# Optimization experiments

Measured on AMD Instinct MI355X. Metric: run time of the kernel, lower is better.

## Reference

```python
import jax, jax.numpy as jnp
import numpy as np

T = 2048        # num tokens
HID = 2048      # hidden_size
HQ = 16         # num_heads
HKV = 8         # num_kv_heads
D = 128         # head_dim
P = 2           # power retention exponent
THETA = 10000.0 # rope base
SCALE = D ** -0.5


def setup_inputs() -> dict:
    key = jax.random.key(0)
    ks = jax.random.split(key, 8)
    s = 0.02
    return {
        "positions": jnp.arange(T, dtype=jnp.int64) if jax.config.jax_enable_x64 else jnp.arange(T, dtype=jnp.int32),
        "hidden_states": jax.random.normal(ks[0], (T, HID), jnp.float32),
        "Wq": jax.random.normal(ks[1], (HID, HQ * D), jnp.float32) * s,
        "bq": jnp.zeros((HQ * D,), jnp.float32),
        "Wk": jax.random.normal(ks[2], (HID, HKV * D), jnp.float32) * s,
        "bk": jnp.zeros((HKV * D,), jnp.float32),
        "Wv": jax.random.normal(ks[3], (HID, HKV * D), jnp.float32) * s,
        "bv": jnp.zeros((HKV * D,), jnp.float32),
        "Wg": jax.random.normal(ks[4], (HID, HKV), jnp.float32) * s,
        "bg": jnp.zeros((HKV,), jnp.float32),
        "Wo": jax.random.normal(ks[5], (HQ * D, HID), jnp.float32) * s,
        "bo": jnp.zeros((HID,), jnp.float32),
    }


def _rope_neox(x, pos):
    # x: [T, H, D], pos: [T]; rotate-half (neox) style, rotary_dim == head_dim
    half = D // 2
    inv_freq = 1.0 / (THETA ** (jnp.arange(0, D, 2, dtype=jnp.float32) / D))  # [D/2]
    freqs = pos.astype(jnp.float32)[:, None] * inv_freq                        # [T, D/2]
    cos = jnp.cos(freqs)[:, None, :]
    sin = jnp.sin(freqs)[:, None, :]
    x1, x2 = x[..., :half], x[..., half:]
    return jnp.concatenate([x1 * cos - x2 * sin, x2 * cos + x1 * sin], axis=-1)


def reference(positions, hidden_states, Wq, bq, Wk, bk, Wv, bv, Wg, bg, Wo, bo):
    # QKVG projections
    q = (hidden_states @ Wq + bq).reshape(T, HQ, D)
    k = (hidden_states @ Wk + bk).reshape(T, HKV, D)
    v = (hidden_states @ Wv + bv).reshape(T, HKV, D)
    g = hidden_states @ Wg + bg            # [T, HKV], one gate scalar per kv head

    # RoPE on q/k, logsigmoid gate in fp32
    q = _rope_neox(q, positions)
    k = _rope_neox(k, positions)
    g = jax.nn.log_sigmoid(g.astype(jnp.float32))   # [T, HKV], <= 0
    G = jnp.cumsum(g, axis=0)                       # [T, HKV] cumulative log-decay

    # GQA: expand kv heads to query heads
    rep = HQ // HKV
    k = jnp.repeat(k, rep, axis=1)   # [T, HQ, D]
    v = jnp.repeat(v, rep, axis=1)
    G = jnp.repeat(G, rep, axis=1)   # [T, HQ]

    # Power retention (quadratic attention form, seq_len <= switch_over_seq_len):
    # W_ij = (scale * q_i . k_j)^p * exp(G_i - G_j), causal j <= i
    S = jnp.einsum('thd,shd->hts', q, k) * SCALE      # [H, T, T]
    S = S ** P
    Gh = G.T                                          # [H, T]
    mask = jnp.tril(jnp.ones((T, T), dtype=bool))
    diff = jnp.where(mask[None], Gh[:, :, None] - Gh[:, None, :], -jnp.inf)
    W = S * jnp.exp(diff)                             # decay<=1 inside mask, 0 outside

    out = jnp.einsum('hts,shd->thd', W, v)            # [T, H, D]
    out = out.reshape(T, HQ * D) @ Wo + bo            # o_proj
    return out
```

## Files before the change

kernel.cpp:

```cpp
#include <hip/hip_runtime.h>
#include <hip/hip_bf16.h>
#include <math.h>

#define T_SEQ 2048
#define HID 2048
#define HQ 16
#define HKV 8
#define D_HEAD 128
#define HALF 64
#define SCALE_F 0.08838834764831845f
#define PROJW 4096

typedef __attribute__((ext_vector_type(8))) short bf16x8;
typedef __attribute__((ext_vector_type(4))) float f32x4;

static __device__ __forceinline__ short f2bf(float x) {
  unsigned u = __builtin_bit_cast(unsigned, x);
  unsigned r = (u + 0x7FFF + ((u >> 16) & 1)) >> 16;
  return (short)r;
}
static __device__ __forceinline__ float bf2f(unsigned short u) {
  unsigned v = ((unsigned)u) << 16;
  return __builtin_bit_cast(float, v);
}

#define GLDS(gsrc, ldst) \
  __builtin_amdgcn_global_load_lds((const __attribute__((address_space(1))) void*)(gsrc), \
                                   (__attribute__((address_space(3))) void*)(ldst), 16, 0, 0)

__global__ __launch_bounds__(256)
void transpose_all(const float* __restrict__ Wq, const float* __restrict__ Wk,
                   const float* __restrict__ Wv, const float* __restrict__ Wo,
                   short* __restrict__ BTall, short* __restrict__ WoT)
{
  const int bx = blockIdx.x;
  const int k0 = blockIdx.y * 32;
  const float* src; short* dst; int Nsrc, n0;
  if (bx < 64)       { src = Wq; Nsrc = 2048; dst = BTall;                       n0 = bx * 32; }
  else if (bx < 96)  { src = Wk; Nsrc = 1024; dst = BTall + (size_t)2048 * 2048; n0 = (bx - 64) * 32; }
  else if (bx < 128) { src = Wv; Nsrc = 1024; dst = BTall + (size_t)3072 * 2048; n0 = (bx - 96) * 32; }
  else               { src = Wo; Nsrc = 2048; dst = WoT;                         n0 = (bx - 128) * 32; }

  __shared__ float tile[32][33];
  const int r = threadIdx.x >> 5, c = threadIdx.x & 31;
  #pragma unroll
  for (int i = 0; i < 4; ++i)
    tile[r + i * 8][c] = src[(size_t)(k0 + r + i * 8) * Nsrc + n0 + c];
  __syncthreads();
  const int n = threadIdx.x >> 3, k4 = (threadIdx.x & 7) * 4;
  short4 o;
  o.x = f2bf(tile[k4 + 0][n]); o.y = f2bf(tile[k4 + 1][n]);
  o.z = f2bf(tile[k4 + 2][n]); o.w = f2bf(tile[k4 + 3][n]);
  *reinterpret_cast<short4*>(&dst[(size_t)(n0 + n) * 2048 + k0 + k4]) = o;
}

__global__ __launch_bounds__(256)
void add_f32(float* __restrict__ out, const float* __restrict__ part, int n4)
{
  int i = blockIdx.x * blockDim.x + threadIdx.x;
  if (i >= n4) return;
  float4 a = reinterpret_cast<float4*>(out)[i];
  const float4 b = reinterpret_cast<const float4*>(part)[i];
  a.x += b.x; a.y += b.y; a.z += b.z; a.w += b.w;
  reinterpret_cast<float4*>(out)[i] = a;
}

template <bool OBF>
__global__ __launch_bounds__(256, 1)
void gemmF(const short* __restrict__ A, const short* __restrict__ BT,
           const float* __restrict__ b0, const float* __restrict__ b1,
           const float* __restrict__ b2, int s1, int s2,
           void* __restrict__ Cout0, void* __restrict__ Cout1,
           int N, int Kst, int klen)
{
  __shared__ short Al[3][256 * 64];
  __shared__ short Bl[3][128 * 64];
  const int tid = threadIdx.x, wid = tid >> 6, lane = tid & 63;
  const int z = blockIdx.z;
  const int koff = z * klen;
  const int nwg = gridDim.x * gridDim.y;
  const int orig = blockIdx.y * gridDim.x + blockIdx.x;
  const int swz = (orig & 7) * (nwg >> 3) + (orig >> 3);
  const int bx = swz % gridDim.x, by = swz / gridDim.x;
  const int bm0 = by * 256, bn0 = bx * 128;
  const int wr = wid >> 1, wc = wid & 1;
  const int c = lane & 15, g = lane >> 4;
  const int xc = (c & 7) << 4;
  const int nk = klen >> 6;

  f32x4 acc[8][4] = {};

#define STGA(p, kt, j) do {                                                   \
    const int cid = (j) * 256 + tid;                                          \
    const int rr = cid >> 3;                                                  \
    const int gx = (cid & 7) ^ (rr & 7);                                      \
    GLDS(A + (size_t)(bm0 + rr) * Kst + koff + (kt) * 64 + gx * 8,            \
         (char*)&Al[p][0] + ((j) * 256 + wid * 64) * 16);                     \
  } while (0)
#define STGB(p, kt, j) do {                                                   \
    const int cid = (j) * 256 + tid;                                          \
    const int rr = cid >> 3;                                                  \
    const int gx = (cid & 7) ^ (rr & 7);                                      \
    GLDS(BT + (size_t)(bn0 + rr) * Kst + koff + (kt) * 64 + gx * 8,           \
         (char*)&Bl[p][0] + ((j) * 256 + wid * 64) * 16);                     \
  } while (0)
#define STAGE(p, kt) do {                                                     \
    STGA(p, kt, 0); STGA(p, kt, 1); STGA(p, kt, 2); STGA(p, kt, 3);           \
    STGA(p, kt, 4); STGA(p, kt, 5); STGA(p, kt, 6); STGA(p, kt, 7);           \
    STGB(p, kt, 0); STGB(p, kt, 1); STGB(p, kt, 2); STGB(p, kt, 3);           \
  } while (0)

#define RDA(p, mf, ks)                                                        \
  (*reinterpret_cast<const bf16x8*>((const char*)&Al[p][0] +                  \
      (size_t)(wr * 128 + (mf) * 16 + c) * 128 + (((ks) * 64 + g * 16) ^ xc)))
#define RDB(p, nf, ks)                                                        \
  (*reinterpret_cast<const bf16x8*>((const char*)&Bl[p][0] +                  \
      (size_t)(wc * 64 + (nf) * 16 + c) * 128 + (((ks) * 64 + g * 16) ^ xc)))

  STAGE(0, 0);
  if (nk > 1) {
    STAGE(1, 1);
    asm volatile("s_waitcnt vmcnt(12)" ::: "memory");
  } else {
    asm volatile("s_waitcnt vmcnt(0)" ::: "memory");
  }
  __builtin_amdgcn_s_barrier();
  __builtin_amdgcn_sched_barrier(0);

  for (int t = 0; t < nk; ++t) {
    const int p = t % 3, sb = (t + 2) % 3;
    if (t + 2 < nk) STAGE(sb, t + 2);

    bf16x8 a0[8], br0[4];
    #pragma unroll
    for (int mf = 0; mf < 8; ++mf) a0[mf] = RDA(p, mf, 0);
    #pragma unroll
    for (int nf = 0; nf < 4; ++nf) br0[nf] = RDB(p, nf, 0);
    asm volatile("s_waitcnt lgkmcnt(0)" ::: "memory");
    __builtin_amdgcn_sched_barrier(0);

    bf16x8 a1[8], br1[4];
    #pragma unroll
    for (int mf = 0; mf < 8; ++mf) a1[mf] = RDA(p, mf, 1);
    #pragma unroll
    for (int nf = 0; nf < 4; ++nf) br1[nf] = RDB(p, nf, 1);
    __builtin_amdgcn_sched_barrier(0);

    __builtin_amdgcn_s_setprio(1);
    #pragma unroll
    for (int mf = 0; mf < 8; ++mf)
      #pragma unroll
      for (int nf = 0; nf < 4; ++nf)
        acc[mf][nf] = __builtin_amdgcn_mfma_f32_16x16x32_bf16(a0[mf], br0[nf], acc[mf][nf], 0, 0, 0);
    __builtin_amdgcn_s_setprio(0);

    asm volatile("s_waitcnt lgkmcnt(0)" ::: "memory");
    __builtin_amdgcn_sched_barrier(0);

    __builtin_amdgcn_s_setprio(1);
    #pragma unroll
    for (int mf = 0; mf < 8; ++mf)
      #pragma unroll
      for (int nf = 0; nf < 4; ++nf)
        acc[mf][nf] = __builtin_amdgcn_mfma_f32_16x16x32_bf16(a1[mf], br1[nf], acc[mf][nf], 0, 0, 0);
    __builtin_amdgcn_s_setprio(0);

    if (t + 1 < nk) {
      __builtin_amdgcn_sched_barrier(0);
      if (t + 2 < nk) asm volatile("s_waitcnt vmcnt(12)" ::: "memory");
      else            asm volatile("s_waitcnt vmcnt(0)" ::: "memory");
      __builtin_amdgcn_s_barrier();
      __builtin_amdgcn_sched_barrier(0);
    }
  }

  void* Cout = z ? Cout1 : Cout0;
  const int crow = bm0 + wr * 128 + g * 4;
  const int ccol = bn0 + wc * 64 + c;
  #pragma unroll
  for (int nf = 0; nf < 4; ++nf) {
    const int col = ccol + nf * 16;
    float b = 0.f;
    if (z == 0)
      b = (col < s1) ? b0[col] : ((col < s2) ? b1[col - s1] : b2[col - s2]);
    #pragma unroll
    for (int mf = 0; mf < 8; ++mf)
      #pragma unroll
      for (int r = 0; r < 4; ++r) {
        const int row = crow + mf * 16 + r;
        const float v = acc[mf][nf][r] + b;
        if constexpr (OBF)
          ((short*)Cout)[(size_t)row * N + col] = f2bf(v);
        else
          ((float*)Cout)[(size_t)row * N + col] = v;
      }
  }
#undef STGA
#undef STGB
#undef STAGE
#undef RDA
#undef RDB
}

__global__ __launch_bounds__(256)
void gproj_kernel(const float* __restrict__ hs, const float* __restrict__ Wg,
                  const float* __restrict__ bg, float* __restrict__ gT,
                  short* __restrict__ hsb)
{
  const int t = blockIdx.x, tid = threadIdx.x;
  __shared__ float red[256][9];
  float a[8] = {0.f, 0.f, 0.f, 0.f, 0.f, 0.f, 0.f, 0.f};
  for (int cc = tid; cc < HID; cc += 256) {
    const float hv = hs[(size_t)t * HID + cc];
    hsb[(size_t)t * HID + cc] = f2bf(hv);
    const float4 w0 = *reinterpret_cast<const float4*>(Wg + (size_t)cc * 8);
    const float4 w1 = *reinterpret_cast<const float4*>(Wg + (size_t)cc * 8 + 4);
    a[0] = fmaf(hv, w0.x, a[0]); a[1] = fmaf(hv, w0.y, a[1]);
    a[2] = fmaf(hv, w0.z, a[2]); a[3] = fmaf(hv, w0.w, a[3]);
    a[4] = fmaf(hv, w1.x, a[4]); a[5] = fmaf(hv, w1.y, a[5]);
    a[6] = fmaf(hv, w1.z, a[6]); a[7] = fmaf(hv, w1.w, a[7]);
  }
  #pragma unroll
  for (int j = 0; j < 8; ++j) red[tid][j] = a[j];
  __syncthreads();
  for (int s = 128; s >= 1; s >>= 1) {
    if (tid < s) {
      #pragma unroll
      for (int j = 0; j < 8; ++j) red[tid][j] += red[tid + s][j];
    }
    __syncthreads();
  }
  if (tid < 8) {
    const float x = red[0][tid] + bg[tid];
    const float nx = -x;
    const float sp = (nx > 20.f) ? nx : log1pf(expf(nx));
    gT[(size_t)tid * T_SEQ + t] = -sp;
  }
}

__global__ __launch_bounds__(512)
void gscan_kernel(const float* __restrict__ gT, float* __restrict__ Gct)
{
  const int h = blockIdx.x;
  const int tid = threadIdx.x;
  const int wid = tid >> 6, lane = tid & 63;
  __shared__ float wsum[8];

  const float4 v = reinterpret_cast<const float4*>(gT + (size_t)h * T_SEQ)[tid];
  const float p0 = v.x, p1 = p0 + v.y, p2 = p1 + v.z, p3 = p2 + v.w;

  float sc = p3;
  #pragma unroll
  for (int off = 1; off < 64; off <<= 1) {
    const float o = __shfl_up(sc, off, 64);
    if (lane >= off) sc += o;
  }
  if (lane == 63) wsum[wid] = sc;
  __syncthreads();
  float wof = 0.f;
  #pragma unroll
  for (int w = 0; w < 8; ++w) wof += (w < wid) ? wsum[w] : 0.f;

  const float excl = wof + sc - p3;
  reinterpret_cast<float4*>(Gct + (size_t)h * T_SEQ)[tid] =
      make_float4(excl + p0, excl + p1, excl + p2, excl + p3);
}

__global__ __launch_bounds__(256)
void rope_vtrans(short* __restrict__ proj, unsigned short* __restrict__ vt)
{
  __shared__ float cs[64], sn[64];
  __shared__ unsigned short tile[32][33];

  if (blockIdx.x < 2048) {
    const int t = blockIdx.x;
    if (threadIdx.x < 64) {
      const int i = threadIdx.x;
      const float f = (float)t * powf(10000.0f, -(float)i / 64.0f);
      cs[i] = cosf(f); sn[i] = sinf(f);
    }
    __syncthreads();
    const int u = threadIdx.x;
    if (u < 192) {
      const int hh = u >> 3, ch = u & 7;
      short* base = proj + (size_t)t * PROJW +
                    ((hh < HQ) ? hh * D_HEAD : 2048 + (hh - HQ) * D_HEAD);
      bf16x8 x1 = *reinterpret_cast<bf16x8*>(base + ch * 8);
      bf16x8 x2 = *reinterpret_cast<bf16x8*>(base + HALF + ch * 8);
      #pragma unroll
      for (int j = 0; j < 8; ++j) {
        const float a = bf2f((unsigned short)x1[j]);
        const float b = bf2f((unsigned short)x2[j]);
        const float cc = cs[ch * 8 + j], ss = sn[ch * 8 + j];
        x1[j] = f2bf(a * cc - b * ss);
        x2[j] = f2bf(b * cc + a * ss);
      }
      *reinterpret_cast<bf16x8*>(base + ch * 8) = x1;
      *reinterpret_cast<bf16x8*>(base + HALF + ch * 8) = x2;
    }
  } else {
    const int idx = blockIdx.x - 2048;
    const int tt = (idx & 63) * 32, dd = ((idx >> 6) & 3) * 32, hk = idx >> 8;
    const unsigned short* pj = (const unsigned short*)proj;
    const int c = threadIdx.x & 31, r0 = (threadIdx.x >> 5) * 4;
    #pragma unroll
    for (int i = 0; i < 4; ++i)
      tile[r0 + i][c] = pj[(size_t)(tt + r0 + i) * PROJW + 3072 + hk * 128 + dd + c];
    __syncthreads();
    #pragma unroll
    for (int i = 0; i < 4; ++i)
      vt[(size_t)(hk * 128 + dd + r0 + i) * T_SEQ + tt + c] = tile[c][r0 + i];
  }
}

__global__ __launch_bounds__(256, 1)
void attn_mfma(const short* __restrict__ proj, const short* __restrict__ vt,
               const float* __restrict__ Gct, short* __restrict__ outb)
{
  __shared__ __align__(16) char smem[86528];
  const int hk = blockIdx.x;
  const int tb = blockIdx.y * 64;
  const int tid = threadIdx.x;
  const int wid = tid >> 6, lane = tid & 63;
  const int c = lane & 15, g = lane >> 4;
  const int h = 2 * hk + (wid >> 1);
  const int tw = tb + (wid & 1) * 32;
  const float* Gh = Gct + (size_t)hk * T_SEQ;

  const float glim = Gh[tb] + 90.0f;
  int lo = 0, hi = tb;
  while (lo < hi) {
    const int mid = (lo + hi) >> 1;
    if (Gh[mid] > glim) lo = mid + 1; else hi = mid;
  }
  const int sfirst = lo & ~63;
  const int nst = ((tb - sfirst) >> 6) + 1;

  bf16x8 qf[2][4];
  #pragma unroll
  for (int tt = 0; tt < 2; ++tt)
    #pragma unroll
    for (int kb = 0; kb < 4; ++kb)
      qf[tt][kb] = *reinterpret_cast<const bf16x8*>(
          proj + (size_t)(tw + 16 * tt + c) * PROJW + h * D_HEAD + kb * 32 + g * 8);
  const float gt0 = Gh[tw + c];
  const float gt1 = Gh[tw + 16 + c];
  const float gtw = Gh[tw];
  const int twmax = tw + 31;

  f32x4 accv[2][8] = {};

#define ASTG(buf, s64)                                                                   \
  do {                                                                                   \
    _Pragma("unroll")                                                                    \
    for (int i2 = 0; i2 < 4; ++i2) {                                                     \
      const int cid = tid + 256 * i2;                                                    \
      const int kr = cid >> 4, kc = cid & 15;                                            \
      GLDS(proj + (size_t)((s64) + kr) * PROJW + 2048 + hk * 128 + ((kc ^ (kr & 7)) * 8),\
           smem + (buf) * 16384 + cid * 16);                                             \
      const int vr = cid >> 3, vc = cid & 7;                                             \
      GLDS(vt + (size_t)(hk * 128 + vr) * T_SEQ + (s64) + ((vc ^ (vr & 7)) * 8),         \
           smem + 32768 + (buf) * 16384 + cid * 16);                                     \
    }                                                                                    \
    if (tid < 64) ((float*)(smem + 86016))[(buf) * 64 + tid] = Gh[(s64) + tid];          \
  } while (0)

  ASTG(0, sfirst);
  __syncthreads();

  for (int i = 0; i < nst; ++i) {
    const int cur = i & 1;
    if (i + 1 < nst) ASTG(cur ^ 1, sfirst + (i + 1) * 64);
    const int sbase64 = sfirst + i * 64;
    const float* Gss = (const float*)(smem + 86016) + cur * 64;
    char* Pmy = smem + 65536 + wid * 5120;

    #pragma unroll
    for (int st = 0; st < 2; ++st) {
      const int s0 = sbase64 + st * 32;
      if (s0 > twmax) continue;
      if (gtw - Gss[st * 32 + 31] < -90.0f) continue;

      bf16x8 kf[2][4];
      #pragma unroll
      for (int sg = 0; sg < 2; ++sg)
        #pragma unroll
        for (int kb = 0; kb < 4; ++kb) {
          const int row = st * 32 + 16 * sg + c;
          const int byt = (row * 256 + kb * 64 + g * 16) ^ ((c & 7) << 4);
          kf[sg][kb] = *reinterpret_cast<const bf16x8*>(smem + cur * 16384 + byt);
        }
      f32x4 sa[2][2] = {};
      #pragma unroll
      for (int kb = 0; kb < 4; ++kb)
        #pragma unroll
        for (int sg = 0; sg < 2; ++sg)
          #pragma unroll
          for (int tt = 0; tt < 2; ++tt)
            sa[sg][tt] = __builtin_amdgcn_mfma_f32_16x16x32_bf16(
                kf[sg][kb], qf[tt][kb], sa[sg][tt], 0, 0, 0);

      #pragma unroll
      for (int sg = 0; sg < 2; ++sg) {
        const float4 gs = *reinterpret_cast<const float4*>(&Gss[st * 32 + sg * 16 + g * 4]);
        const float gsv[4] = {gs.x, gs.y, gs.z, gs.w};
        #pragma unroll
        for (int tt = 0; tt < 2; ++tt) {
          const int tg = tw + 16 * tt + c;
          const float gt = tt ? gt1 : gt0;
          const int sg0 = s0 + sg * 16 + g * 4;
          float w[4];
          #pragma unroll
          for (int r = 0; r < 4; ++r) {
            const float dv = sa[sg][tt][r] * SCALE_F;
            const float ww = dv * dv * __expf(gt - gsv[r]);
            w[r] = (sg0 + r <= tg) ? ww : 0.0f;
          }
          uint2 pv;
          pv.x = ((unsigned)(unsigned short)f2bf(w[1]) << 16) | (unsigned short)f2bf(w[0]);
          pv.y = ((unsigned)(unsigned short)f2bf(w[3]) << 16) | (unsigned short)f2bf(w[2]);
          *reinterpret_cast<uint2*>(Pmy + st * 2560 + (c + 16 * tt) * 80 + 8 * g + 32 * sg) = pv;
        }
      }
      asm volatile("s_waitcnt lgkmcnt(0)" ::: "memory");
      __builtin_amdgcn_sched_barrier(0);

      bf16x8 pf[2];
      #pragma unroll
      for (int tt = 0; tt < 2; ++tt)
        pf[tt] = *reinterpret_cast<const bf16x8*>(Pmy + st * 2560 + (c + 16 * tt) * 80 + g * 16);

      #pragma unroll
      for (int db = 0; db < 8; ++db) {
        const int row = 16 * db + c;
        const int byt = (row * 128 + st * 64 + g * 16) ^ ((c & 7) << 4);
        const bf16x8 vf = *reinterpret_cast<const bf16x8*>(smem + 32768 + cur * 16384 + byt);
        #pragma unroll
        for (int tt = 0; tt < 2; ++tt)
          accv[tt][db] = __builtin_amdgcn_mfma_f32_16x16x32_bf16(pf[tt], vf, accv[tt][db], 0, 0, 0);
      }
    }
    __syncthreads();
  }

  char* Wme = smem + wid * 8704;
  #pragma unroll
  for (int tt = 0; tt < 2; ++tt)
    #pragma unroll
    for (int db = 0; db < 8; ++db)
      #pragma unroll
      for (int r = 0; r < 4; ++r)
        *reinterpret_cast<short*>(Wme + (16 * tt + 4 * g + r) * 272 + (16 * db + c) * 2)
            = f2bf(accv[tt][db][r]);
  asm volatile("s_waitcnt lgkmcnt(0)" ::: "memory");
  __builtin_amdgcn_sched_barrier(0);
  #pragma unroll
  for (int e = 0; e < 8; ++e) {
    const int idx = e * 64 + lane;
    const int tr = idx >> 4, d0 = (idx & 15) * 8;
    const bf16x8 vv = *reinterpret_cast<const bf16x8*>(Wme + tr * 272 + d0 * 2);
    *reinterpret_cast<bf16x8*>(outb + ((size_t)(tw + tr) * HQ + h) * D_HEAD + d0) = vv;
  }
#undef ASTG
}

extern "C" void kernel_launch(void* const* d_in, const int* in_sizes, int n_in,
                              void* d_out, int out_size, void* d_ws, size_t ws_size,
                              hipStream_t stream)
{
  const float* hs = (const float*)d_in[1];
  const float* Wq = (const float*)d_in[2];
  const float* bq = (const float*)d_in[3];
  const float* Wk = (const float*)d_in[4];
  const float* bk = (const float*)d_in[5];
  const float* Wv = (const float*)d_in[6];
  const float* bv = (const float*)d_in[7];
  const float* Wg = (const float*)d_in[8];
  const float* bg = (const float*)d_in[9];
  const float* Wo = (const float*)d_in[10];
  const float* bo = (const float*)d_in[11];
  float* outp = (float*)d_out;

  short* proj  = (short*)d_ws;
  short* vtb   = proj + (size_t)T_SEQ * PROJW;
  float* gT    = (float*)(vtb + (size_t)HKV * D_HEAD * T_SEQ);
  float* Gct   = gT + 16384;
  short* hsb   = (short*)(Gct + 16384);
  short* BTall = hsb + (size_t)2048 * 2048;
  short* WoT   = BTall + (size_t)4096 * 2048;
  short* attnout = hsb;
  float* opart   = (float*)BTall;

  transpose_all<<<dim3(192, 64), 256, 0, stream>>>(Wq, Wk, Wv, Wo, BTall, WoT);

  gproj_kernel<<<2048, 256, 0, stream>>>(hs, Wg, bg, gT, hsb);
  gscan_kernel<<<8, 512, 0, stream>>>(gT, Gct);

  gemmF<true><<<dim3(32, 8, 1), 256, 0, stream>>>(
      hsb, BTall, bq, bk, bv, 2048, 3072, proj, proj, PROJW, 2048, 2048);

  rope_vtrans<<<4096, 256, 0, stream>>>(proj, (unsigned short*)vtb);

  attn_mfma<<<dim3(8, 32), 256, 0, stream>>>(proj, vtb, Gct, attnout);

  gemmF<false><<<dim3(16, 8, 2), 256, 0, stream>>>(
      attnout, WoT, bo, bo, bo, 1 << 30, 1 << 30, outp, opart, 2048, 2048, 1024);
  add_f32<<<4096, 256, 0, stream>>>(outp, opart, 1048576);
}
```

Measured before the change: 152.5 us.

## Use 256x256 split-K GEMM tiles with bf16 partials and fused fold+RoPE

```diff
diff --git a/kernel.cpp b/kernel.cpp
--- a/kernel.cpp
+++ b/kernel.cpp
@@ -29,17 +29,15 @@
                                    (__attribute__((address_space(3))) void*)(ldst), 16, 0, 0)
 
 __global__ __launch_bounds__(256)
-void transpose_all(const float* __restrict__ Wq, const float* __restrict__ Wk,
-                   const float* __restrict__ Wv, const float* __restrict__ Wo,
-                   short* __restrict__ BTall, short* __restrict__ WoT)
+void transpose_qkvw(const float* __restrict__ Wq, const float* __restrict__ Wk,
+                    const float* __restrict__ Wv, short* __restrict__ BTall)
 {
   const int bx = blockIdx.x;
   const int k0 = blockIdx.y * 32;
   const float* src; short* dst; int Nsrc, n0;
   if (bx < 64)       { src = Wq; Nsrc = 2048; dst = BTall;                       n0 = bx * 32; }
   else if (bx < 96)  { src = Wk; Nsrc = 1024; dst = BTall + (size_t)2048 * 2048; n0 = (bx - 64) * 32; }
-  else if (bx < 128) { src = Wv; Nsrc = 1024; dst = BTall + (size_t)3072 * 2048; n0 = (bx - 96) * 32; }
-  else               { src = Wo; Nsrc = 2048; dst = WoT;                         n0 = (bx - 128) * 32; }
+  else               { src = Wv; Nsrc = 1024; dst = BTall + (size_t)3072 * 2048; n0 = (bx - 96) * 32; }
 
   __shared__ float tile[32][33];
   const int r = threadIdx.x >> 5, c = threadIdx.x & 31;
@@ -55,35 +53,41 @@
 }
 
 __global__ __launch_bounds__(256)
-void add_f32(float* __restrict__ out, const float* __restrict__ part, int n4)
-{
-  int i = blockIdx.x * blockDim.x + threadIdx.x;
-  if (i >= n4) return;
-  float4 a = reinterpret_cast<float4*>(out)[i];
-  const float4 b = reinterpret_cast<const float4*>(part)[i];
-  a.x += b.x; a.y += b.y; a.z += b.z; a.w += b.w;
-  reinterpret_cast<float4*>(out)[i] = a;
-}
-
-template <bool OBF>
-__global__ __launch_bounds__(256, 1)
-void gemmF(const short* __restrict__ A, const short* __restrict__ BT,
-           const float* __restrict__ b0, const float* __restrict__ b1,
-           const float* __restrict__ b2, int s1, int s2,
-           void* __restrict__ Cout0, void* __restrict__ Cout1,
-           int N, int Kst, int klen)
-{
-  __shared__ short Al[3][256 * 64];
-  __shared__ short Bl[3][128 * 64];
+void transpose_wo(const float* __restrict__ Wo, short* __restrict__ WoT)
+{
+  const int k0 = blockIdx.y * 32, n0 = blockIdx.x * 32;
+  __shared__ float tile[32][33];
+  const int r = threadIdx.x >> 5, c = threadIdx.x & 31;
+  #pragma unroll
+  for (int i = 0; i < 4; ++i)
+    tile[r + i * 8][c] = Wo[(size_t)(k0 + r + i * 8) * 2048 + n0 + c];
+  __syncthreads();
+  const int n = threadIdx.x >> 3, k4 = (threadIdx.x & 7) * 4;
+  short4 o;
+  o.x = f2bf(tile[k4 + 0][n]); o.y = f2bf(tile[k4 + 1][n]);
+  o.z = f2bf(tile[k4 + 2][n]); o.w = f2bf(tile[k4 + 3][n]);
+  *reinterpret_cast<short4*>(&WoT[(size_t)(n0 + n) * 2048 + k0 + k4]) = o;
+}
+
+template <bool OBF0>
+__global__ __launch_bounds__(512, 1)
+void gemm256(const short* __restrict__ A, const short* __restrict__ BT,
+             const float* __restrict__ b0, const float* __restrict__ b1,
+             const float* __restrict__ b2, int s1, int s2,
+             void* __restrict__ C0, short* __restrict__ P1,
+             short* __restrict__ P2, short* __restrict__ P3,
+             int N, int Kst, int klen)
+{
+  __shared__ __align__(16) short Al[2][256 * 64];
+  __shared__ __align__(16) short Bl[2][256 * 64];
   const int tid = threadIdx.x, wid = tid >> 6, lane = tid & 63;
-  const int z = blockIdx.z;
-  const int koff = z * klen;
+  const int z = blockIdx.z, koff = z * klen;
   const int nwg = gridDim.x * gridDim.y;
   const int orig = blockIdx.y * gridDim.x + blockIdx.x;
   const int swz = (orig & 7) * (nwg >> 3) + (orig >> 3);
   const int bx = swz % gridDim.x, by = swz / gridDim.x;
-  const int bm0 = by * 256, bn0 = bx * 128;
-  const int wr = wid >> 1, wc = wid & 1;
+  const int bm0 = by * 256, bn0 = bx * 256;
+  const int wr = wid >> 2, wc = wid & 3;
   const int c = lane & 15, g = lane >> 4;
   const int xc = (c & 7) << 4;
   const int nk = klen >> 6;
@@ -91,22 +95,21 @@
   f32x4 acc[8][4] = {};
 
 #define STGA(p, kt, j) do {                                                   \
-    const int cid = (j) * 256 + tid;                                          \
+    const int cid = (j) * 512 + tid;                                          \
     const int rr = cid >> 3;                                                  \
     const int gx = (cid & 7) ^ (rr & 7);                                      \
     GLDS(A + (size_t)(bm0 + rr) * Kst + koff + (kt) * 64 + gx * 8,            \
-         (char*)&Al[p][0] + ((j) * 256 + wid * 64) * 16);                     \
+         (char*)&Al[p][0] + ((j) * 512 + wid * 64) * 16);                     \
   } while (0)
 #define STGB(p, kt, j) do {                                                   \
-    const int cid = (j) * 256 + tid;                                          \
+    const int cid = (j) * 512 + tid;                                          \
     const int rr = cid >> 3;                                                  \
     const int gx = (cid & 7) ^ (rr & 7);                                      \
     GLDS(BT + (size_t)(bn0 + rr) * Kst + koff + (kt) * 64 + gx * 8,           \
-         (char*)&Bl[p][0] + ((j) * 256 + wid * 64) * 16);                     \
+         (char*)&Bl[p][0] + ((j) * 512 + wid * 64) * 16);                     \
   } while (0)
 #define STAGE(p, kt) do {                                                     \
     STGA(p, kt, 0); STGA(p, kt, 1); STGA(p, kt, 2); STGA(p, kt, 3);           \
-    STGA(p, kt, 4); STGA(p, kt, 5); STGA(p, kt, 6); STGA(p, kt, 7);           \
     STGB(p, kt, 0); STGB(p, kt, 1); STGB(p, kt, 2); STGB(p, kt, 3);           \
   } while (0)
 
@@ -118,81 +121,78 @@
       (size_t)(wc * 64 + (nf) * 16 + c) * 128 + (((ks) * 64 + g * 16) ^ xc)))
 
   STAGE(0, 0);
-  if (nk > 1) {
-    STAGE(1, 1);
-    asm volatile("s_waitcnt vmcnt(12)" ::: "memory");
-  } else {
-    asm volatile("s_waitcnt vmcnt(0)" ::: "memory");
-  }
+  asm volatile("s_waitcnt vmcnt(0)" ::: "memory");
   __builtin_amdgcn_s_barrier();
   __builtin_amdgcn_sched_barrier(0);
 
   for (int t = 0; t < nk; ++t) {
-    const int p = t % 3, sb = (t + 2) % 3;
-    if (t + 2 < nk) STAGE(sb, t + 2);
-
-    bf16x8 a0[8], br0[4];
-    #pragma unroll
-    for (int mf = 0; mf < 8; ++mf) a0[mf] = RDA(p, mf, 0);
-    #pragma unroll
-    for (int nf = 0; nf < 4; ++nf) br0[nf] = RDB(p, nf, 0);
-    asm volatile("s_waitcnt lgkmcnt(0)" ::: "memory");
-    __builtin_amdgcn_sched_barrier(0);
-
-    bf16x8 a1[8], br1[4];
-    #pragma unroll
-    for (int mf = 0; mf < 8; ++mf) a1[mf] = RDA(p, mf, 1);
-    #pragma unroll
-    for (int nf = 0; nf < 4; ++nf) br1[nf] = RDB(p, nf, 1);
-    __builtin_amdgcn_sched_barrier(0);
-
-    __builtin_amdgcn_s_setprio(1);
-    #pragma unroll
-    for (int mf = 0; mf < 8; ++mf)
-      #pragma unroll
-      for (int nf = 0; nf < 4; ++nf)
-        acc[mf][nf] = __builtin_amdgcn_mfma_f32_16x16x32_bf16(a0[mf], br0[nf], acc[mf][nf], 0, 0, 0);
-    __builtin_amdgcn_s_setprio(0);
-
-    asm volatile("s_waitcnt lgkmcnt(0)" ::: "memory");
-    __builtin_amdgcn_sched_barrier(0);
-
-    __builtin_amdgcn_s_setprio(1);
-    #pragma unroll
-    for (int mf = 0; mf < 8; ++mf)
-      #pragma unroll
-      for (int nf = 0; nf < 4; ++nf)
-        acc[mf][nf] = __builtin_amdgcn_mfma_f32_16x16x32_bf16(a1[mf], br1[nf], acc[mf][nf], 0, 0, 0);
-    __builtin_amdgcn_s_setprio(0);
+    const int p = t & 1;
+    if (t + 1 < nk) STAGE(p ^ 1, t + 1);
+
+    {
+      bf16x8 af[8], bfr[4];
+      #pragma unroll
+      for (int mf = 0; mf < 8; ++mf) af[mf] = RDA(p, mf, 0);
+      #pragma unroll
+      for (int nf = 0; nf < 4; ++nf) bfr[nf] = RDB(p, nf, 0);
+      asm volatile("s_waitcnt lgkmcnt(0)" ::: "memory");
+      __builtin_amdgcn_sched_barrier(0);
+      __builtin_amdgcn_s_setprio(1);
+      #pragma unroll
+      for (int mf = 0; mf < 8; ++mf)
+        #pragma unroll
+        for (int nf = 0; nf < 4; ++nf)
+          acc[mf][nf] = __builtin_amdgcn_mfma_f32_16x16x32_bf16(af[mf], bfr[nf], acc[mf][nf], 0, 0, 0);
+      __builtin_amdgcn_s_setprio(0);
+    }
+    {
+      bf16x8 af[8], bfr[4];
+      #pragma unroll
+      for (int mf = 0; mf < 8; ++mf) af[mf] = RDA(p, mf, 1);
+      #pragma unroll
+      for (int nf = 0; nf < 4; ++nf) bfr[nf] = RDB(p, nf, 1);
+      asm volatile("s_waitcnt lgkmcnt(0)" ::: "memory");
+      __builtin_amdgcn_sched_barrier(0);
+      __builtin_amdgcn_s_setprio(1);
+      #pragma unroll
+      for (int mf = 0; mf < 8; ++mf)
+        #pragma unroll
+        for (int nf = 0; nf < 4; ++nf)
+          acc[mf][nf] = __builtin_amdgcn_mfma_f32_16x16x32_bf16(af[mf], bfr[nf], acc[mf][nf], 0, 0, 0);
+      __builtin_amdgcn_s_setprio(0);
+    }
 
     if (t + 1 < nk) {
       __builtin_amdgcn_sched_barrier(0);
-      if (t + 2 < nk) asm volatile("s_waitcnt vmcnt(12)" ::: "memory");
-      else            asm volatile("s_waitcnt vmcnt(0)" ::: "memory");
+      asm volatile("s_waitcnt vmcnt(0)" ::: "memory");
       __builtin_amdgcn_s_barrier();
       __builtin_amdgcn_sched_barrier(0);
     }
   }
 
-  void* Cout = z ? Cout1 : Cout0;
-  const int crow = bm0 + wr * 128 + g * 4;
-  const int ccol = bn0 + wc * 64 + c;
+  const int crow = bm0 + wr * 128;
+  const int ccol0 = bn0 + wc * 64;
   #pragma unroll
   for (int nf = 0; nf < 4; ++nf) {
-    const int col = ccol + nf * 16;
+    const int col = ccol0 + nf * 16 + c;
     float b = 0.f;
     if (z == 0)
       b = (col < s1) ? b0[col] : ((col < s2) ? b1[col - s1] : b2[col - s2]);
+    short* P = (z == 1) ? P1 : ((z == 2) ? P2 : P3);
     #pragma unroll
     for (int mf = 0; mf < 8; ++mf)
       #pragma unroll
       for (int r = 0; r < 4; ++r) {
-        const int row = crow + mf * 16 + r;
+        const int row = crow + mf * 16 + g * 4 + r;
         const float v = acc[mf][nf][r] + b;
-        if constexpr (OBF)
-          ((short*)Cout)[(size_t)row * N + col] = f2bf(v);
-        else
-          ((float*)Cout)[(size_t)row * N + col] = v;
+        if (z == 0) {
+          if constexpr (OBF0)
+            ((short*)C0)[(size_t)row * N + col] = f2bf(v);
+          else
+            ((float*)C0)[(size_t)row * N + col] = v;
+        } else {
+          P[(size_t)row * N + col] = f2bf(v);
+        }
       }
   }
 #undef STGA
@@ -267,50 +267,75 @@
 }
 
 __global__ __launch_bounds__(256)
-void rope_vtrans(short* __restrict__ proj, unsigned short* __restrict__ vt)
-{
+void qkv_fold_rope(short* __restrict__ proj, const short* __restrict__ part1)
+{
+  const int t = blockIdx.x;
   __shared__ float cs[64], sn[64];
+  if (threadIdx.x < 64) {
+    const int i = threadIdx.x;
+    const float f = (float)t * powf(10000.0f, -(float)i / 64.0f);
+    cs[i] = cosf(f); sn[i] = sinf(f);
+  }
+  __syncthreads();
+
+  const int ch = ((threadIdx.x >> 3) << 4) + (threadIdx.x & 7);
+  const size_t base = (size_t)t * PROJW + ch * 8;
+  bf16x8 a1 = *reinterpret_cast<bf16x8*>(proj + base);
+  bf16x8 a2 = *reinterpret_cast<bf16x8*>(proj + base + 64);
+  const bf16x8 q1 = *reinterpret_cast<const bf16x8*>(part1 + base);
+  const bf16x8 q2 = *reinterpret_cast<const bf16x8*>(part1 + base + 64);
+  const int head = ch >> 4;
+  const int i0 = (ch & 7) * 8;
+  #pragma unroll
+  for (int j = 0; j < 8; ++j) {
+    const float x1 = bf2f((unsigned short)a1[j]) + bf2f((unsigned short)q1[j]);
+    const float x2 = bf2f((unsigned short)a2[j]) + bf2f((unsigned short)q2[j]);
+    if (head < 24) {
+      const float cc = cs[i0 + j], ss = sn[i0 + j];
+      a1[j] = f2bf(x1 * cc - x2 * ss);
+      a2[j] = f2bf(x2 * cc + x1 * ss);
+    } else {
+      a1[j] = f2bf(x1);
+      a2[j] = f2bf(x2);
+    }
+  }
+  *reinterpret_cast<bf16x8*>(proj + base) = a1;
+  *reinterpret_cast<bf16x8*>(proj + base + 64) = a2;
+}
+
+__global__ __launch_bounds__(256)
+void vtrans_kernel(const unsigned short* __restrict__ proj, unsigned short* __restrict__ vt)
+{
   __shared__ unsigned short tile[32][33];
-
-  if (blockIdx.x < 2048) {
-    const int t = blockIdx.x;
-    if (threadIdx.x < 64) {
-      const int i = threadIdx.x;
-      const float f = (float)t * powf(10000.0f, -(float)i / 64.0f);
-      cs[i] = cosf(f); sn[i] = sinf(f);
-    }
-    __syncthreads();
-    const int u = threadIdx.x;
-    if (u < 192) {
-      const int hh = u >> 3, ch = u & 7;
-      short* base = proj + (size_t)t * PROJW +
-                    ((hh < HQ) ? hh * D_HEAD : 2048 + (hh - HQ) * D_HEAD);
-      bf16x8 x1 = *reinterpret_cast<bf16x8*>(base + ch * 8);
-      bf16x8 x2 = *reinterpret_cast<bf16x8*>(base + HALF + ch * 8);
-      #pragma unroll
-      for (int j = 0; j < 8; ++j) {
-        const float a = bf2f((unsigned short)x1[j]);
-        const float b = bf2f((unsigned short)x2[j]);
-        const float cc = cs[ch * 8 + j], ss = sn[ch * 8 + j];
-        x1[j] = f2bf(a * cc - b * ss);
-        x2[j] = f2bf(b * cc + a * ss);
-      }
-      *reinterpret_cast<bf16x8*>(base + ch * 8) = x1;
-      *reinterpret_cast<bf16x8*>(base + HALF + ch * 8) = x2;
-    }
-  } else {
-    const int idx = blockIdx.x - 2048;
-    const int tt = (idx & 63) * 32, dd = ((idx >> 6) & 3) * 32, hk = idx >> 8;
-    const unsigned short* pj = (const unsigned short*)proj;
-    const int c = threadIdx.x & 31, r0 = (threadIdx.x >> 5) * 4;
-    #pragma unroll
-    for (int i = 0; i < 4; ++i)
-      tile[r0 + i][c] = pj[(size_t)(tt + r0 + i) * PROJW + 3072 + hk * 128 + dd + c];
-    __syncthreads();
-    #pragma unroll
-    for (int i = 0; i < 4; ++i)
-      vt[(size_t)(hk * 128 + dd + r0 + i) * T_SEQ + tt + c] = tile[c][r0 + i];
-  }
+  const int tt = blockIdx.x * 32, dd = blockIdx.y * 32, hk = blockIdx.z;
+  const int c = threadIdx.x & 31, r0 = (threadIdx.x >> 5) * 4;
+  #pragma unroll
+  for (int i = 0; i < 4; ++i)
+    tile[r0 + i][c] = proj[(size_t)(tt + r0 + i) * PROJW + 3072 + hk * 128 + dd + c];
+  __syncthreads();
+  #pragma unroll
+  for (int i = 0; i < 4; ++i)
+    vt[(size_t)(hk * 128 + dd + r0 + i) * T_SEQ + tt + c] = tile[c][r0 + i];
+}
+
+__global__ __launch_bounds__(256)
+void o_fold(float* __restrict__ out, const short* __restrict__ p1,
+            const short* __restrict__ p2, const short* __restrict__ p3)
+{
+  const size_t i = ((size_t)blockIdx.x * 256 + threadIdx.x) * 8;
+  const bf16x8 a = *reinterpret_cast<const bf16x8*>(p1 + i);
+  const bf16x8 b = *reinterpret_cast<const bf16x8*>(p2 + i);
+  const bf16x8 cc = *reinterpret_cast<const bf16x8*>(p3 + i);
+  float4 o0 = *reinterpret_cast<float4*>(out + i);
+  float4 o1 = *reinterpret_cast<float4*>(out + i + 4);
+  float s[8];
+  #pragma unroll
+  for (int j = 0; j < 8; ++j)
+    s[j] = bf2f((unsigned short)a[j]) + bf2f((unsigned short)b[j]) + bf2f((unsigned short)cc[j]);
+  o0.x += s[0]; o0.y += s[1]; o0.z += s[2]; o0.w += s[3];
+  o1.x += s[4]; o1.y += s[5]; o1.z += s[6]; o1.w += s[7];
+  *reinterpret_cast<float4*>(out + i) = o0;
+  *reinterpret_cast<float4*>(out + i + 4) = o1;
 }
 
 __global__ __launch_bounds__(256, 1)
@@ -487,23 +512,34 @@
   float* Gct   = gT + 16384;
   short* hsb   = (short*)(Gct + 16384);
   short* BTall = hsb + (size_t)2048 * 2048;
-  short* WoT   = BTall + (size_t)4096 * 2048;
+  short* part1 = BTall + (size_t)4096 * 2048;
+  short* WoT     = BTall;
   short* attnout = hsb;
-  float* opart   = (float*)BTall;
-
-  transpose_all<<<dim3(192, 64), 256, 0, stream>>>(Wq, Wk, Wv, Wo, BTall, WoT);
+  short* opart1  = part1;
+  short* opart2  = part1 + (size_t)2048 * 2048;
+  short* opart3  = proj;
+
+  transpose_qkvw<<<dim3(128, 64), 256, 0, stream>>>(Wq, Wk, Wv, BTall);
 
   gproj_kernel<<<2048, 256, 0, stream>>>(hs, Wg, bg, gT, hsb);
   gscan_kernel<<<8, 512, 0, stream>>>(gT, Gct);
 
-  gemmF<true><<<dim3(32, 8, 1), 256, 0, stream>>>(
-      hsb, BTall, bq, bk, bv, 2048, 3072, proj, proj, PROJW, 2048, 2048);
-
-  rope_vtrans<<<4096, 256, 0, stream>>>(proj, (unsigned short*)vtb);
+  gemm256<true><<<dim3(16, 8, 2), 512, 0, stream>>>(
+      hsb, BTall, bq, bk, bv, 2048, 3072, proj, part1, part1, part1,
+      PROJW, 2048, 1024);
+
+  qkv_fold_rope<<<2048, 256, 0, stream>>>(proj, part1);
+
+  vtrans_kernel<<<dim3(64, 4, 8), 256, 0, stream>>>((const unsigned short*)proj,
+                                                    (unsigned short*)vtb);
+
+  transpose_wo<<<dim3(64, 64), 256, 0, stream>>>(Wo, WoT);
 
   attn_mfma<<<dim3(8, 32), 256, 0, stream>>>(proj, vtb, Gct, attnout);
 
-  gemmF<false><<<dim3(16, 8, 2), 256, 0, stream>>>(
-      attnout, WoT, bo, bo, bo, 1 << 30, 1 << 30, outp, opart, 2048, 2048, 1024);
-  add_f32<<<4096, 256, 0, stream>>>(outp, opart, 1048576);
-}
+  gemm256<false><<<dim3(8, 8, 4), 512, 0, stream>>>(
+      attnout, WoT, bo, bo, bo, 1 << 30, 1 << 30, outp, opart1, opart2, opart3,
+      2048, 2048, 512);
+
+  o_fold<<<2048, 256, 0, stream>>>(outp, opart1, opart2, opart3);
+}
```

Result: faster. 145.1 us (-4.9%).
